# Kernel optimization log

Hardware: AMD Instinct MI355X
Metric: run time of the kernel (lower is better)

The kernel has to match this reference:

```python
import jax, jax.numpy as jnp
import numpy as np

N = 4096          # batch size
D = 1024          # embedding dim
NUM_INSTANCES = 8 # samples per class (balanced batch, required by the original resize logic)
ALPHA = 20.0
MARGIN = 0.5


def setup_inputs() -> dict:
    key = jax.random.key(0)
    inputs = jax.random.normal(key, (N, D), dtype=jnp.float32)
    # balanced targets: each class appears exactly NUM_INSTANCES times
    targets = (jnp.arange(N, dtype=jnp.int32) // NUM_INSTANCES).astype(jnp.int32)
    return {"inputs": inputs, "targets": targets}


def reference(inputs, targets):
    n = inputs.shape[0]
    k_pos = NUM_INSTANCES - 1          # positives per row (excl. self)
    k_neg = n - NUM_INSTANCES          # negatives per row

    # L2 normalize rows, cosine similarity matrix [n, n]
    x = inputs / jnp.linalg.norm(inputs, axis=1, keepdims=True)
    sim = x @ x.T

    same = targets[:, None] == targets[None, :]
    eye = jnp.eye(n, dtype=bool)
    pos_mask = same & ~eye             # positives, diag removed
    neg_mask = ~same                   # negatives

    INF = jnp.float32(1e9)
    # per-row sorted positive / negative sims (ascending); fixed-size slices
    pos_sorted = jnp.sort(jnp.where(pos_mask, sim, INF), axis=1)[:, :k_pos]   # [n, k_pos]
    neg_sorted = jnp.sort(jnp.where(neg_mask, sim, INF), axis=1)[:, :k_neg]   # [n, k_neg]

    # base = max(max(sim) - 0.1, margin + 0.2)
    base = jnp.maximum(jnp.max(sim) - 0.1, MARGIN + 0.2)

    # dynamic selection expressed as masks over fixed-size sorted arrays
    neg_keep = neg_sorted > (pos_sorted[:, :1] - 0.05)   # negatives above min positive - 0.05
    pos_keep = pos_sorted < base                          # positives below base

    pos_elem = jnp.log1p(jnp.exp(-2.0 * (pos_sorted - MARGIN)))   # [n, k_pos]
    neg_elem = jnp.log1p(jnp.exp(ALPHA * (neg_sorted - MARGIN)))  # [n, k_neg]

    pos_cnt = pos_keep.sum(axis=1)
    neg_cnt = neg_keep.sum(axis=1)

    pos_mean = (pos_elem * pos_keep).sum(axis=1) / jnp.maximum(pos_cnt, 1).astype(sim.dtype)
    neg_mean = (neg_elem * neg_keep).sum(axis=1) / jnp.maximum(neg_cnt, 1).astype(sim.dtype)

    # fallbacks: empty pos set -> smallest positive; empty neg set -> largest negative
    pos_loss = jnp.where(pos_cnt > 0, pos_mean, pos_elem[:, 0])
    neg_loss = jnp.where(neg_cnt > 0, neg_mean, neg_elem[:, -1])

    return jnp.mean(pos_loss + neg_loss)   # sum over rows / n
```

## Files before the change

kernel.cpp:

```cpp
#include <hip/hip_runtime.h>
#include <hip/hip_bf16.h>
#include <math.h>

#define N 4096
#define D 1024
#define NINST 8
#define NGROUP (N / NINST)
#define ALPHA 20.0f
#define MARGIN 0.5f
#define NB 64
#define NTILE (NB * (NB + 1) / 2)

typedef __attribute__((ext_vector_type(8))) short bf16x8;
typedef __attribute__((ext_vector_type(4))) float f32x4;

__device__ __forceinline__ unsigned fkey(float f) {
    int b = __float_as_int(f);
    return (b >= 0) ? ((unsigned)b | 0x80000000u) : ~(unsigned)b;
}
__device__ __forceinline__ float fdec(unsigned u) {
    int b = (u & 0x80000000u) ? (int)(u ^ 0x80000000u) : ~(int)u;
    return __int_as_float(b);
}

__device__ __forceinline__ float softplus(float x) {
    float z = __expf(-fabsf(x));
    return fmaxf(x, 0.0f) + __logf(1.0f + z);
}

__device__ __forceinline__ void gld16(const void* g, void* l) {
    __builtin_amdgcn_global_load_lds(
        (const __attribute__((address_space(1))) void*)g,
        (__attribute__((address_space(3))) void*)l, 16, 0, 0);
}

__global__ __launch_bounds__(256) void k_normpos(const float* __restrict__ in,
                                                 ushort* __restrict__ xn,
                                                 float* __restrict__ pos_sims,
                                                 float* __restrict__ min_pos,
                                                 unsigned* __restrict__ gmax,
                                                 float* __restrict__ accum,
                                                 unsigned* __restrict__ cnt) {
    __shared__ float4 srows4[8 * 257];
    __shared__ float spart[8][4];
    __shared__ float sinv[8];
    __shared__ float sg[8][8];

    int g = blockIdx.x;
    int t = threadIdx.x;
    int lane = t & 63, wid = t >> 6;

    if (g == 0 && t == 0) { *gmax = 0u; *accum = 0.f; *cnt = 0u; }

    const float4* in4 = (const float4*)in;
    #pragma unroll
    for (int i = 0; i < 8; ++i) {
        float4 v = in4[(size_t)g * 2048 + i * 256 + t];
        srows4[i * 257 + t] = v;
        float ss = v.x * v.x + v.y * v.y + v.z * v.z + v.w * v.w;
        #pragma unroll
        for (int off = 1; off < 64; off <<= 1) ss += __shfl_xor(ss, off);
        if (lane == 0) spart[i][wid] = ss;
    }
    __syncthreads();
    if (t < 8) sinv[t] = rsqrtf(spart[t][0] + spart[t][1] + spart[t][2] + spart[t][3]);
    __syncthreads();

    #pragma unroll
    for (int i = 0; i < 8; ++i) {
        float4 v = srows4[i * 257 + t];
        float inv = sinv[i];
        ushort4 o;
        __hip_bfloat16 h;
        h = __float2bfloat16(v.x * inv); o.x = *(ushort*)&h;
        h = __float2bfloat16(v.y * inv); o.y = *(ushort*)&h;
        h = __float2bfloat16(v.z * inv); o.z = *(ushort*)&h;
        h = __float2bfloat16(v.w * inv); o.w = *(ushort*)&h;
        ((ushort4*)(xn + (size_t)(g * 8 + i) * D))[t] = o;
    }

    int pair = t >> 2, a = pair >> 3, b = pair & 7, slice = t & 3;
    const float4* pa = srows4 + a * 257 + slice * 64;
    const float4* pb = srows4 + b * 257 + slice * 64;
    float s = 0.f;
    #pragma unroll 8
    for (int i = 0; i < 64; ++i) {
        float4 x = pa[i], y = pb[i];
        s += x.x * y.x + x.y * y.y + x.z * y.z + x.w * y.w;
    }
    s += __shfl_xor(s, 1);
    s += __shfl_xor(s, 2);
    if (slice == 0) sg[a][b] = s * sinv[a] * sinv[b];
    __syncthreads();
    if (t < 8) {
        float mn = 1e30f;
        int idx = 0;
        #pragma unroll
        for (int b2 = 0; b2 < 8; ++b2) {
            if (b2 == t) continue;
            float v = sg[t][b2];
            mn = fminf(mn, v);
            pos_sims[(size_t)(g * 8 + t) * 8 + idx] = v;
            ++idx;
        }
        min_pos[g * 8 + t] = mn;
    }
}

__global__ __launch_bounds__(64, 2) void k_neg(const ushort* __restrict__ xn,
                                               const float* __restrict__ min_pos,
                                               float* __restrict__ sum_part,
                                               int* __restrict__ cnt_part,
                                               float* __restrict__ max_part,
                                               unsigned* __restrict__ gmax) {
    __shared__ ushort sA[2][64 * 32];
    __shared__ ushort sB[2][64 * 32];

    int bid = blockIdx.x;
    int rt = 0, rem = bid;
    while (rem >= NB - rt) { rem -= NB - rt; ++rt; }
    int ct = rt + rem;
    bool diag = (rt == ct);

    int R0 = rt * 64, C0 = ct * 64;
    int l = threadIdx.x;
    int lrow = l & 15;
    int kgrp = l >> 4;

    float mA = min_pos[R0 + l];
    float mB = min_pos[C0 + l];

    const ushort* gA = xn + (size_t)(R0 + (l >> 2)) * D + (l & 3) * 8;
    const ushort* gB = xn + (size_t)(C0 + (l >> 2)) * D + (l & 3) * 8;

    f32x4 zero = {0.f, 0.f, 0.f, 0.f};
    f32x4 acc[4][4];
    #pragma unroll
    for (int m = 0; m < 4; ++m)
        #pragma unroll
        for (int n = 0; n < 4; ++n) acc[m][n] = zero;

    #define STAGE(buf, k0)                                               \
        do {                                                             \
            char* lA_ = (char*)sA[buf];                                  \
            char* lB_ = (char*)sB[buf];                                  \
            gld16(gA + (k0),            lA_);                            \
            gld16(gA + (k0) + 16 * D,   lA_ + 1024);                     \
            gld16(gA + (k0) + 32 * D,   lA_ + 2048);                     \
            gld16(gA + (k0) + 48 * D,   lA_ + 3072);                     \
            gld16(gB + (k0),            lB_);                            \
            gld16(gB + (k0) + 16 * D,   lB_ + 1024);                     \
            gld16(gB + (k0) + 32 * D,   lB_ + 2048);                     \
            gld16(gB + (k0) + 48 * D,   lB_ + 3072);                     \
        } while (0)

    STAGE(0, 0);
    STAGE(1, 32);

    for (int it = 0; it < 32; ++it) {
        if (it < 31) asm volatile("s_waitcnt vmcnt(8)" ::: "memory");
        else         asm volatile("s_waitcnt vmcnt(0)" ::: "memory");

        int cur = it & 1;
        const ushort* fA = sA[cur] + (size_t)lrow * 32 + kgrp * 8;
        const ushort* fB = sB[cur] + (size_t)lrow * 32 + kgrp * 8;
        bf16x8 a[4], b[4];
        #pragma unroll
        for (int m = 0; m < 4; ++m)
            a[m] = *(const bf16x8*)(fA + (size_t)m * 16 * 32);
        #pragma unroll
        for (int n = 0; n < 4; ++n)
            b[n] = *(const bf16x8*)(fB + (size_t)n * 16 * 32);

        asm volatile("s_waitcnt lgkmcnt(0)" ::: "memory");
        if (it <= 29) STAGE(cur, (it + 2) * 32);

        #pragma unroll
        for (int m = 0; m < 4; ++m)
            #pragma unroll
            for (int n = 0; n < 4; ++n)
                acc[m][n] = __builtin_amdgcn_mfma_f32_16x16x32_bf16(a[m], b[n], acc[m][n], 0, 0, 0);
    }
    #undef STAGE

    float allmax = -1e30f;

    float thB[4];
    #pragma unroll
    for (int n = 0; n < 4; ++n) thB[n] = __shfl(mB, n * 16 + lrow) - 0.05f;

    float colS[4] = {0.f, 0.f, 0.f, 0.f};
    float colM[4] = {-1e30f, -1e30f, -1e30f, -1e30f};
    int   colC[4] = {0, 0, 0, 0};

    #pragma unroll
    for (int m = 0; m < 4; ++m) {
        #pragma unroll
        for (int reg = 0; reg < 4; ++reg) {
            int lr = m * 16 + kgrp * 4 + reg;
            int grow = R0 + lr;
            float th = __shfl(mA, lr) - 0.05f;
            int gi = grow >> 3;
            float rs = 0.f, rm = -1e30f;
            int rc = 0;
            #pragma unroll
            for (int n = 0; n < 4; ++n) {
                int gcol = C0 + n * 16 + lrow;
                float s = acc[m][n][reg];
                allmax = fmaxf(allmax, s);
                if ((gcol >> 3) != gi) {
                    float e = softplus(ALPHA * (s - MARGIN));
                    rm = fmaxf(rm, s);
                    if (s > th) { rs += e; rc += 1; }
                    if (!diag) {
                        colM[n] = fmaxf(colM[n], s);
                        if (s > thB[n]) { colS[n] += e; colC[n] += 1; }
                    }
                }
            }
            #pragma unroll
            for (int off = 1; off < 16; off <<= 1) {
                rs += __shfl_xor(rs, off);
                rc += __shfl_xor(rc, off);
                rm = fmaxf(rm, __shfl_xor(rm, off));
            }
            if (lrow == 0) {
                sum_part[(size_t)grow * 64 + ct] = rs;
                cnt_part[(size_t)grow * 64 + ct] = rc;
                max_part[(size_t)grow * 64 + ct] = rm;
            }
        }
    }

    if (!diag) {
        #pragma unroll
        for (int n = 0; n < 4; ++n) {
            float cs = colS[n], cm = colM[n];
            int cc = colC[n];
            cs += __shfl_xor(cs, 16); cs += __shfl_xor(cs, 32);
            cc += __shfl_xor(cc, 16); cc += __shfl_xor(cc, 32);
            cm = fmaxf(cm, __shfl_xor(cm, 16));
            cm = fmaxf(cm, __shfl_xor(cm, 32));
            if (kgrp == 0) {
                int gcol = C0 + n * 16 + lrow;
                sum_part[(size_t)gcol * 64 + rt] = cs;
                cnt_part[(size_t)gcol * 64 + rt] = cc;
                max_part[(size_t)gcol * 64 + rt] = cm;
            }
        }
    }

    #pragma unroll
    for (int off = 1; off < 64; off <<= 1) allmax = fmaxf(allmax, __shfl_xor(allmax, off));
    if (l == 0) atomicMax(gmax, fkey(allmax));
}

__global__ __launch_bounds__(256) void k_rowfinal(const float* __restrict__ sum_part,
                                                  const int* __restrict__ cnt_part,
                                                  const float* __restrict__ max_part,
                                                  const float* __restrict__ pos_sims,
                                                  const float* __restrict__ min_pos,
                                                  const unsigned* __restrict__ gmax,
                                                  float* __restrict__ accum,
                                                  unsigned* __restrict__ cnt,
                                                  float* __restrict__ out) {
    __shared__ float sloss[4];
    int row = blockIdx.x * 4 + (threadIdx.x >> 6);
    int lane = threadIdx.x & 63;
    float ns = sum_part[(size_t)row * 64 + lane];
    int nc = cnt_part[(size_t)row * 64 + lane];
    float nm = max_part[(size_t)row * 64 + lane];
    #pragma unroll
    for (int off = 1; off < 64; off <<= 1) {
        ns += __shfl_xor(ns, off);
        nc += __shfl_xor(nc, off);
        nm = fmaxf(nm, __shfl_xor(nm, off));
    }
    if (lane == 0) {
        float base = fmaxf(fdec(*gmax) - 0.1f, MARGIN + 0.2f);
        float neg_loss = (nc > 0) ? ns / (float)nc : softplus(ALPHA * (nm - MARGIN));
        float ps = 0.f;
        int pcnt = 0;
        float mn = min_pos[row];
        #pragma unroll
        for (int i = 0; i < NINST - 1; ++i) {
            float s = pos_sims[(size_t)row * 8 + i];
            if (s < base) { ps += softplus(-2.0f * (s - MARGIN)); pcnt++; }
        }
        float pos_loss = (pcnt > 0) ? ps / (float)pcnt : softplus(-2.0f * (mn - MARGIN));
        sloss[threadIdx.x >> 6] = pos_loss + neg_loss;
    }
    __syncthreads();
    if (threadIdx.x == 0) {
        float bs = sloss[0] + sloss[1] + sloss[2] + sloss[3];
        atomicAdd(accum, bs);
        __threadfence();
        unsigned old = atomicAdd(cnt, 1u);
        if (old == gridDim.x - 1) {
            __threadfence();
            float tot = atomicAdd(accum, 0.0f);
            out[0] = tot / (float)N;
        }
    }
}

extern "C" void kernel_launch(void* const* d_in, const int* in_sizes, int n_in,
                              void* d_out, int out_size, void* d_ws, size_t ws_size,
                              hipStream_t stream) {
    const float* in = (const float*)d_in[0];
    float* out = (float*)d_out;

    char* ws = (char*)d_ws;
    ushort*  xn       = (ushort*)(ws);
    float*   min_pos  = (float*)(ws + 8388608 + 16384);
    float*   pos_sims = (float*)(ws + 8388608 + 32768);
    float*   sum_part = (float*)(ws + 8388608 + 32768 + 131072);
    float*   max_part = (float*)(ws + 8388608 + 32768 + 131072 + 1048576);
    int*     cnt_part = (int*)  (ws + 8388608 + 32768 + 131072 + 2097152);
    unsigned* gmax    = (unsigned*)(ws + 8388608 + 32768 + 131072 + 3145728);
    float*   accum    = (float*)(ws + 8388608 + 32768 + 131072 + 3145728 + 64);
    unsigned* cnt     = (unsigned*)(ws + 8388608 + 32768 + 131072 + 3145728 + 128);

    k_normpos<<<NGROUP, 256, 0, stream>>>(in, xn, pos_sims, min_pos, gmax, accum, cnt);
    k_neg<<<NTILE, 64, 0, stream>>>(xn, min_pos, sum_part, cnt_part, max_part, gmax);
    k_rowfinal<<<N / 4, 256, 0, stream>>>(sum_part, cnt_part, max_part, pos_sims, min_pos,
                                          gmax, accum, cnt, out);
}
```

Baseline: 120.1 us.

## Switch similarity GEMM to FP8 MFMA with direct register loads

Normalized embeddings are now stored as FP8 e4m3 instead of bf16, and the negative-similarity tile GEMM uses the fp8 16x16x32 MFMA. The LDS double-buffered global_load_lds staging is replaced by direct 8-byte global loads into registers with a two-stage software prefetch. This halves operand bytes and the matrix work per MFMA. The cost is much lower precision in the cosine similarities, which feed sharp thresholds and an exp with ALPHA=20, so the loss value may drift beyond tolerance.

```diff
diff --git a/kernel.cpp b/kernel.cpp
--- a/kernel.cpp
+++ b/kernel.cpp
@@ -1,5 +1,6 @@
 #include <hip/hip_runtime.h>
 #include <hip/hip_bf16.h>
+#include <hip/hip_fp8.h>
 #include <math.h>
 
 #define N 4096
@@ -11,7 +12,6 @@
 #define NB 64
 #define NTILE (NB * (NB + 1) / 2)
 
-typedef __attribute__((ext_vector_type(8))) short bf16x8;
 typedef __attribute__((ext_vector_type(4))) float f32x4;
 
 __device__ __forceinline__ unsigned fkey(float f) {
@@ -28,14 +28,8 @@
     return fmaxf(x, 0.0f) + __logf(1.0f + z);
 }
 
-__device__ __forceinline__ void gld16(const void* g, void* l) {
-    __builtin_amdgcn_global_load_lds(
-        (const __attribute__((address_space(1))) void*)g,
-        (__attribute__((address_space(3))) void*)l, 16, 0, 0);
-}
-
 __global__ __launch_bounds__(256) void k_normpos(const float* __restrict__ in,
-                                                 ushort* __restrict__ xn,
+                                                 unsigned char* __restrict__ xn8,
                                                  float* __restrict__ pos_sims,
                                                  float* __restrict__ min_pos,
                                                  unsigned* __restrict__ gmax,
@@ -70,13 +64,12 @@
     for (int i = 0; i < 8; ++i) {
         float4 v = srows4[i * 257 + t];
         float inv = sinv[i];
-        ushort4 o;
-        __hip_bfloat16 h;
-        h = __float2bfloat16(v.x * inv); o.x = *(ushort*)&h;
-        h = __float2bfloat16(v.y * inv); o.y = *(ushort*)&h;
-        h = __float2bfloat16(v.z * inv); o.z = *(ushort*)&h;
-        h = __float2bfloat16(v.w * inv); o.w = *(ushort*)&h;
-        ((ushort4*)(xn + (size_t)(g * 8 + i) * D))[t] = o;
+        union { uchar4 u4; unsigned u; } o;
+        o.u4.x = __hip_fp8_e4m3(v.x * inv).__x;
+        o.u4.y = __hip_fp8_e4m3(v.y * inv).__x;
+        o.u4.z = __hip_fp8_e4m3(v.z * inv).__x;
+        o.u4.w = __hip_fp8_e4m3(v.w * inv).__x;
+        ((unsigned*)(xn8 + (size_t)(g * 8 + i) * D))[t] = o.u;
     }
 
     int pair = t >> 2, a = pair >> 3, b = pair & 7, slice = t & 3;
@@ -107,15 +100,12 @@
     }
 }
 
-__global__ __launch_bounds__(64, 2) void k_neg(const ushort* __restrict__ xn,
+__global__ __launch_bounds__(64, 2) void k_neg(const unsigned char* __restrict__ xn8,
                                                const float* __restrict__ min_pos,
                                                float* __restrict__ sum_part,
                                                int* __restrict__ cnt_part,
                                                float* __restrict__ max_part,
                                                unsigned* __restrict__ gmax) {
-    __shared__ ushort sA[2][64 * 32];
-    __shared__ ushort sB[2][64 * 32];
-
     int bid = blockIdx.x;
     int rt = 0, rem = bid;
     while (rem >= NB - rt) { rem -= NB - rt; ++rt; }
@@ -130,8 +120,8 @@
     float mA = min_pos[R0 + l];
     float mB = min_pos[C0 + l];
 
-    const ushort* gA = xn + (size_t)(R0 + (l >> 2)) * D + (l & 3) * 8;
-    const ushort* gB = xn + (size_t)(C0 + (l >> 2)) * D + (l & 3) * 8;
+    const unsigned char* pA = xn8 + (size_t)(R0 + lrow) * D + kgrp * 8;
+    const unsigned char* pB = xn8 + (size_t)(C0 + lrow) * D + kgrp * 8;
 
     f32x4 zero = {0.f, 0.f, 0.f, 0.f};
     f32x4 acc[4][4];
@@ -140,48 +130,36 @@
         #pragma unroll
         for (int n = 0; n < 4; ++n) acc[m][n] = zero;
 
-    #define STAGE(buf, k0)                                               \
-        do {                                                             \
-            char* lA_ = (char*)sA[buf];                                  \
-            char* lB_ = (char*)sB[buf];                                  \
-            gld16(gA + (k0),            lA_);                            \
-            gld16(gA + (k0) + 16 * D,   lA_ + 1024);                     \
-            gld16(gA + (k0) + 32 * D,   lA_ + 2048);                     \
-            gld16(gA + (k0) + 48 * D,   lA_ + 3072);                     \
-            gld16(gB + (k0),            lB_);                            \
-            gld16(gB + (k0) + 16 * D,   lB_ + 1024);                     \
-            gld16(gB + (k0) + 32 * D,   lB_ + 2048);                     \
-            gld16(gB + (k0) + 48 * D,   lB_ + 3072);                     \
+    long a0[4], b0[4], a1[4], b1[4];
+
+    #define LOADF(A, B, k0)                                                   \
+        do {                                                                  \
+            _Pragma("unroll")                                                 \
+            for (int m = 0; m < 4; ++m) {                                     \
+                A[m] = *(const long*)(pA + (size_t)m * 16 * D + (k0) * 32);   \
+                B[m] = *(const long*)(pB + (size_t)m * 16 * D + (k0) * 32);   \
+            }                                                                 \
         } while (0)
 
-    STAGE(0, 0);
-    STAGE(1, 32);
-
-    for (int it = 0; it < 32; ++it) {
-        if (it < 31) asm volatile("s_waitcnt vmcnt(8)" ::: "memory");
-        else         asm volatile("s_waitcnt vmcnt(0)" ::: "memory");
-
-        int cur = it & 1;
-        const ushort* fA = sA[cur] + (size_t)lrow * 32 + kgrp * 8;
-        const ushort* fB = sB[cur] + (size_t)lrow * 32 + kgrp * 8;
-        bf16x8 a[4], b[4];
-        #pragma unroll
-        for (int m = 0; m < 4; ++m)
-            a[m] = *(const bf16x8*)(fA + (size_t)m * 16 * 32);
-        #pragma unroll
-        for (int n = 0; n < 4; ++n)
-            b[n] = *(const bf16x8*)(fB + (size_t)n * 16 * 32);
-
-        asm volatile("s_waitcnt lgkmcnt(0)" ::: "memory");
-        if (it <= 29) STAGE(cur, (it + 2) * 32);
-
-        #pragma unroll
-        for (int m = 0; m < 4; ++m)
-            #pragma unroll
-            for (int n = 0; n < 4; ++n)
-                acc[m][n] = __builtin_amdgcn_mfma_f32_16x16x32_bf16(a[m], b[n], acc[m][n], 0, 0, 0);
-    }
-    #undef STAGE
+    #define MFMAS(A, B)                                                       \
+        do {                                                                  \
+            _Pragma("unroll")                                                 \
+            for (int m = 0; m < 4; ++m)                                       \
+                _Pragma("unroll")                                             \
+                for (int n = 0; n < 4; ++n)                                   \
+                    acc[m][n] = __builtin_amdgcn_mfma_f32_16x16x32_fp8_fp8(   \
+                        A[m], B[n], acc[m][n], 0, 0, 0);                      \
+        } while (0)
+
+    LOADF(a0, b0, 0);
+    for (int it = 0; it < 32; it += 2) {
+        LOADF(a1, b1, it + 1);
+        MFMAS(a0, b0);
+        if (it + 2 < 32) LOADF(a0, b0, it + 2);
+        MFMAS(a1, b1);
+    }
+    #undef LOADF
+    #undef MFMAS
 
     float allmax = -1e30f;
 
@@ -311,7 +289,7 @@
     float* out = (float*)d_out;
 
     char* ws = (char*)d_ws;
-    ushort*  xn       = (ushort*)(ws);
+    unsigned char* xn8 = (unsigned char*)(ws);
     float*   min_pos  = (float*)(ws + 8388608 + 16384);
     float*   pos_sims = (float*)(ws + 8388608 + 32768);
     float*   sum_part = (float*)(ws + 8388608 + 32768 + 131072);
@@ -321,8 +299,8 @@
     float*   accum    = (float*)(ws + 8388608 + 32768 + 131072 + 3145728 + 64);
     unsigned* cnt     = (unsigned*)(ws + 8388608 + 32768 + 131072 + 3145728 + 128);
 
-    k_normpos<<<NGROUP, 256, 0, stream>>>(in, xn, pos_sims, min_pos, gmax, accum, cnt);
-    k_neg<<<NTILE, 64, 0, stream>>>(xn, min_pos, sum_part, cnt_part, max_part, gmax);
+    k_normpos<<<NGROUP, 256, 0, stream>>>(in, xn8, pos_sims, min_pos, gmax, accum, cnt);
+    k_neg<<<NTILE, 64, 0, stream>>>(xn8, min_pos, sum_part, cnt_part, max_part, gmax);
     k_rowfinal<<<N / 4, 256, 0, stream>>>(sum_part, cnt_part, max_part, pos_sims, min_pos,
                                           gmax, accum, cnt, out);
 }
```

Measured after the change: 140.8 us. +17.2%, slower.
